# Kernel optimization log

Measured on AMD Instinct MI355X. Metric: run time of the kernel, lower is better.

## Reference

```python
import jax, jax.numpy as jnp
import numpy as np

N_NODES = 100000
N_EDGES = 3200000
R0, R1, R2, N1 = 16, 8, 16, 32


def setup_inputs() -> dict:
    key = jax.random.key(0)
    ks = jax.random.split(key, 12)
    x = jax.random.normal(ks[0], (N_NODES, R0), dtype=jnp.float32)
    edge_index = jax.random.randint(ks[1], (2, N_EDGES), 0, N_NODES, dtype=jnp.int64)
    s = 0.1
    return {
        "x": x,
        "edge_index": edge_index,
        # GraphConv 1: lin_rel (weight+bias) applied to aggregated neighbors, lin_root (no bias) to self
        "W_rel1": jax.random.normal(ks[2], (R0, R1), dtype=jnp.float32) * s,
        "b_rel1": jnp.zeros((R1,), dtype=jnp.float32),
        "W_root1": jax.random.normal(ks[3], (R0, R1), dtype=jnp.float32) * s,
        # GraphConv 2
        "W_rel2": jax.random.normal(ks[4], (R1, R2), dtype=jnp.float32) * s,
        "b_rel2": jnp.zeros((R2,), dtype=jnp.float32),
        "W_root2": jax.random.normal(ks[5], (R1, R2), dtype=jnp.float32) * s,
        # fc layers
        "W_fc1": jax.random.normal(ks[6], (R2, N1), dtype=jnp.float32) * s,
        "b_fc1": jnp.zeros((N1,), dtype=jnp.float32),
        "W_fc2": jax.random.normal(ks[7], (N1, 1), dtype=jnp.float32) * s,
        "b_fc2": jnp.zeros((1,), dtype=jnp.float32),
    }


def _graph_conv(x, src, dst, W_rel, b_rel, W_root):
    # GraphConv with aggr='add': out_i = lin_rel(sum_{j->i} x_j) + lin_root(x_i)
    agg = jax.ops.segment_sum(x[src], dst, num_segments=N_NODES)  # [N, d_in]
    return agg @ W_rel + b_rel + x @ W_root


def reference(x, edge_index,
              W_rel1, b_rel1, W_root1,
              W_rel2, b_rel2, W_root2,
              W_fc1, b_fc1, W_fc2, b_fc2):
    src, dst = edge_index[0], edge_index[1]
    h = jax.nn.relu(_graph_conv(x, src, dst, W_rel1, b_rel1, W_root1))
    h = jax.nn.relu(_graph_conv(h, src, dst, W_rel2, b_rel2, W_root2))
    h = jax.nn.relu(h @ W_fc1 + b_fc1)
    out = h @ W_fc2 + b_fc2  # [N, 1]
    return out - jnp.mean(out)
```

## Files before the change

kernel.cpp:

```cpp
#include <hip/hip_runtime.h>

#define NN 100000
#define NE 3200000
#define BSH 7
#define BNODES 128
#define NBUCK 782
#define BCAP 4800
#define BIN_CHUNK 8192
#define NBIN_BLOCKS ((NE + BIN_CHUNK - 1) / BIN_CHUNK)
#define NL1_BLOCKS ((NN + 1023) / 1024)
#define NAGG_BLOCKS 1568

#define S1 2097152.0f
#define S2 524288.0f
#define INV_S1 (1.0f / S1)
#define INV_S2 (1.0f / S2)

__global__ __launch_bounds__(1024, 8) void bin_and_l1(
        const float* __restrict__ x,
        const float* __restrict__ Wrel1,
        const float* __restrict__ brel1,
        const float* __restrict__ Wroot1,
        const int* __restrict__ src,
        const int* __restrict__ dst,
        int* __restrict__ y1q,
        int* __restrict__ initq,
        int* __restrict__ bucketCnt,
        int* __restrict__ bpay) {
    int t = threadIdx.x;

    if (blockIdx.x >= NBIN_BLOCKS) {
        __shared__ float sW[16 * 8];
        __shared__ float sR[16 * 8];
        __shared__ float sb[8];
        if (t < 128) { sW[t] = Wrel1[t]; sR[t] = Wroot1[t]; }
        if (t < 8)   { sb[t] = brel1[t]; }
        __syncthreads();

        int i = (blockIdx.x - NBIN_BLOCKS) * 1024 + t;
        if (i >= NN) return;

        const float4* xp = (const float4*)(x + (size_t)i * 16);
        float4 x0 = xp[0], x1 = xp[1], x2 = xp[2], x3 = xp[3];
        float xi[16] = {x0.x, x0.y, x0.z, x0.w, x1.x, x1.y, x1.z, x1.w,
                        x2.x, x2.y, x2.z, x2.w, x3.x, x3.y, x3.z, x3.w};

        float y[8], r[8];
#pragma unroll
        for (int j = 0; j < 8; ++j) { y[j] = 0.0f; r[j] = sb[j]; }
#pragma unroll
        for (int k = 0; k < 16; ++k) {
            float xv = xi[k];
#pragma unroll
            for (int j = 0; j < 8; ++j) {
                y[j] = fmaf(xv, sW[k * 8 + j], y[j]);
                r[j] = fmaf(xv, sR[k * 8 + j], r[j]);
            }
        }
        int4* yp = (int4*)(y1q + (size_t)i * 8);
        int4* ap = (int4*)(initq + (size_t)i * 8);
        int4 q0, q1, p0, p1;
        q0.x = __float2int_rn(y[0] * S1); q0.y = __float2int_rn(y[1] * S1);
        q0.z = __float2int_rn(y[2] * S1); q0.w = __float2int_rn(y[3] * S1);
        q1.x = __float2int_rn(y[4] * S1); q1.y = __float2int_rn(y[5] * S1);
        q1.z = __float2int_rn(y[6] * S1); q1.w = __float2int_rn(y[7] * S1);
        p0.x = __float2int_rn(r[0] * S1); p0.y = __float2int_rn(r[1] * S1);
        p0.z = __float2int_rn(r[2] * S1); p0.w = __float2int_rn(r[3] * S1);
        p1.x = __float2int_rn(r[4] * S1); p1.y = __float2int_rn(r[5] * S1);
        p1.z = __float2int_rn(r[6] * S1); p1.w = __float2int_rn(r[7] * S1);
        yp[0] = q0; yp[1] = q1;
        ap[0] = p0; ap[1] = p1;
        return;
    }

    __shared__ int2 stage2[BIN_CHUNK];
    __shared__ int  hist[NBUCK];
    __shared__ int  gdelta[NBUCK];
    __shared__ int  wsum16[16];

    int e0 = blockIdx.x * BIN_CHUNK;
    int nE = NE - e0; if (nE > BIN_CHUNK) nE = BIN_CHUNK;
    int nv = nE >> 2;

    if (t < NBUCK) hist[t] = 0;
    __syncthreads();

    const int4* dst4 = (const int4*)(dst + e0);
    const int4* src4 = (const int4*)(src + e0);

    int4 d0_, s0_, d1_, s1_;
    bool h0 = (t < nv), h1 = (t + 1024 < nv);
    if (h0) {
        d0_ = dst4[t]; s0_ = src4[t];
        atomicAdd(&hist[d0_.x >> BSH], 1);
        atomicAdd(&hist[d0_.y >> BSH], 1);
        atomicAdd(&hist[d0_.z >> BSH], 1);
        atomicAdd(&hist[d0_.w >> BSH], 1);
    }
    if (h1) {
        d1_ = dst4[t + 1024]; s1_ = src4[t + 1024];
        atomicAdd(&hist[d1_.x >> BSH], 1);
        atomicAdd(&hist[d1_.y >> BSH], 1);
        atomicAdd(&hist[d1_.z >> BSH], 1);
        atomicAdd(&hist[d1_.w >> BSH], 1);
    }
    __syncthreads();

    int c = (t < NBUCK) ? hist[t] : 0;
    int lane = t & 63, w = t >> 6;
    int pref = c;
#pragma unroll
    for (int off = 1; off < 64; off <<= 1) {
        int u = __shfl_up(pref, off);
        if (lane >= off) pref += u;
    }
    if (lane == 63) wsum16[w] = pref;
    __syncthreads();
    if (t < 16) {
        int s = wsum16[t];
#pragma unroll
        for (int off = 1; off < 16; off <<= 1) {
            int u = __shfl_up(s, off);
            if (t >= off) s += u;
        }
        wsum16[t] = s;
    }
    __syncthreads();
    int base = w ? wsum16[w - 1] : 0;
    int excl = base + pref - c;

    if (t < NBUCK) {
        int gb0 = c ? atomicAdd(&bucketCnt[t], c) : 0;
        hist[t] = excl;
        gdelta[t] = t * BCAP + gb0 - excl;
    }
    __syncthreads();

#define PLACE1(dv, sv) do {                                              \
        int b_ = (dv) >> BSH;                                            \
        int r_ = atomicAdd(&hist[b_], 1);                                \
        int ga_ = r_ + gdelta[b_];                                       \
        int2 e_; e_.x = (((dv) & (BNODES - 1)) << 17) | (sv);            \
        e_.y = (ga_ < (b_ + 1) * BCAP) ? ga_ : -1;                       \
        stage2[r_] = e_;                                                 \
    } while (0)

    if (h0) { PLACE1(d0_.x, s0_.x); PLACE1(d0_.y, s0_.y);
              PLACE1(d0_.z, s0_.z); PLACE1(d0_.w, s0_.w); }
    if (h1) { PLACE1(d1_.x, s1_.x); PLACE1(d1_.y, s1_.y);
              PLACE1(d1_.z, s1_.z); PLACE1(d1_.w, s1_.w); }
#undef PLACE1
    __syncthreads();

    for (int p = t; p < nE; p += 1024) {
        int2 e = stage2[p];
        if (e.y >= 0) bpay[e.y] = e.x;
    }
}

__global__ __launch_bounds__(512, 8) void bucket_agg1(const int* __restrict__ bucketCnt,
                                                      const int* __restrict__ bpay,
                                                      const int* __restrict__ y1q,
                                                      int* __restrict__ h1q ) {
    __shared__ int qacc[BNODES * 4];
    int t = threadIdx.x;
    int j = blockIdx.x & 15, kk = blockIdx.x >> 4;
    int b = (kk << 3) + (j & 7);
    int fh4 = (j >> 3) << 2;
    if (b >= NBUCK) return;
    int gb = b * BCAP;
    int fbase = b * (BNODES * 8);

    {
        int node = t >> 2, f = t & 3;
        int gi = fbase + node * 8 + fh4 + f;
        qacc[t] = (gi < NN * 8) ? h1q[gi] : 0;
    }
    int C = bucketCnt[b]; if (C > BCAP) C = BCAP;
    __syncthreads();

    int f = t & 3, g = t >> 2;
    const int4* bp4 = (const int4*)(bpay + gb);
    int iters = C >> 10;
    for (int it = 0; it < iters; ++it) {
        int4 va = bp4[(it << 8) + (g << 1)];
        int4 vb = bp4[(it << 8) + (g << 1) + 1];
        int a0 = y1q[((va.x & 0x1FFFF) << 3) + fh4 + f];
        int a1 = y1q[((va.y & 0x1FFFF) << 3) + fh4 + f];
        int a2 = y1q[((va.z & 0x1FFFF) << 3) + fh4 + f];
        int a3 = y1q[((va.w & 0x1FFFF) << 3) + fh4 + f];
        int a4 = y1q[((vb.x & 0x1FFFF) << 3) + fh4 + f];
        int a5 = y1q[((vb.y & 0x1FFFF) << 3) + fh4 + f];
        int a6 = y1q[((vb.z & 0x1FFFF) << 3) + fh4 + f];
        int a7 = y1q[((vb.w & 0x1FFFF) << 3) + fh4 + f];
        atomicAdd(&qacc[((va.x >> 17) << 2) + f], a0);
        atomicAdd(&qacc[((va.y >> 17) << 2) + f], a1);
        atomicAdd(&qacc[((va.z >> 17) << 2) + f], a2);
        atomicAdd(&qacc[((va.w >> 17) << 2) + f], a3);
        atomicAdd(&qacc[((vb.x >> 17) << 2) + f], a4);
        atomicAdd(&qacc[((vb.y >> 17) << 2) + f], a5);
        atomicAdd(&qacc[((vb.z >> 17) << 2) + f], a6);
        atomicAdd(&qacc[((vb.w >> 17) << 2) + f], a7);
    }
    for (int e = (iters << 10) + g; e < C; e += 128) {
        int v = bpay[gb + e];
        int a = y1q[((v & 0x1FFFF) << 3) + fh4 + f];
        atomicAdd(&qacc[((v >> 17) << 2) + f], a);
    }
    __syncthreads();

    {
        int node = t >> 2, fo = t & 3;
        int gi = fbase + node * 8 + fh4 + fo;
        if (gi < NN * 8) {
            float h = (float)qacc[t] * INV_S1;
            h = h > 0.0f ? h : 0.0f;
            h1q[gi] = __float2int_rn(h * S2);
        }
    }
}

__global__ __launch_bounds__(512, 8) void bucket_agg2(const int* __restrict__ bucketCnt,
                                                      const int* __restrict__ bpay,
                                                      const int* __restrict__ h1q,
                                                      int* __restrict__ sagg) {
    __shared__ int qacc[BNODES * 4];
    int t = threadIdx.x;
    int j = blockIdx.x & 15, kk = blockIdx.x >> 4;
    int b = (kk << 3) + (j & 7);
    int fh4 = (j >> 3) << 2;
    if (b >= NBUCK) return;
    int gb = b * BCAP;
    int fbase = b * (BNODES * 8);

    qacc[t] = 0;
    int C = bucketCnt[b]; if (C > BCAP) C = BCAP;
    __syncthreads();

    int f = t & 3, g = t >> 2;
    const int4* bp4 = (const int4*)(bpay + gb);
    int iters = C >> 10;
    for (int it = 0; it < iters; ++it) {
        int4 va = bp4[(it << 8) + (g << 1)];
        int4 vb = bp4[(it << 8) + (g << 1) + 1];
        int a0 = h1q[((va.x & 0x1FFFF) << 3) + fh4 + f];
        int a1 = h1q[((va.y & 0x1FFFF) << 3) + fh4 + f];
        int a2 = h1q[((va.z & 0x1FFFF) << 3) + fh4 + f];
        int a3 = h1q[((va.w & 0x1FFFF) << 3) + fh4 + f];
        int a4 = h1q[((vb.x & 0x1FFFF) << 3) + fh4 + f];
        int a5 = h1q[((vb.y & 0x1FFFF) << 3) + fh4 + f];
        int a6 = h1q[((vb.z & 0x1FFFF) << 3) + fh4 + f];
        int a7 = h1q[((vb.w & 0x1FFFF) << 3) + fh4 + f];
        atomicAdd(&qacc[((va.x >> 17) << 2) + f], a0);
        atomicAdd(&qacc[((va.y >> 17) << 2) + f], a1);
        atomicAdd(&qacc[((va.z >> 17) << 2) + f], a2);
        atomicAdd(&qacc[((va.w >> 17) << 2) + f], a3);
        atomicAdd(&qacc[((vb.x >> 17) << 2) + f], a4);
        atomicAdd(&qacc[((vb.y >> 17) << 2) + f], a5);
        atomicAdd(&qacc[((vb.z >> 17) << 2) + f], a6);
        atomicAdd(&qacc[((vb.w >> 17) << 2) + f], a7);
    }
    for (int e = (iters << 10) + g; e < C; e += 128) {
        int v = bpay[gb + e];
        int a = h1q[((v & 0x1FFFF) << 3) + fh4 + f];
        atomicAdd(&qacc[((v >> 17) << 2) + f], a);
    }
    __syncthreads();

    {
        int node = t >> 2, fo = t & 3;
        int gi = fbase + node * 8 + fh4 + fo;
        if (gi < NN * 8) sagg[gi] = qacc[t];
    }
}

__global__ __launch_bounds__(512) void dense_tail(const int* __restrict__ h1q,
                                                  const int* __restrict__ sagg,
                                                  const float* __restrict__ Wrel2,
                                                  const float* __restrict__ brel2,
                                                  const float* __restrict__ Wroot2,
                                                  const float* __restrict__ Wfc1,
                                                  const float* __restrict__ bfc1,
                                                  const float* __restrict__ Wfc2,
                                                  const float* __restrict__ bfc2,
                                                  float* __restrict__ out,
                                                  float* __restrict__ gsum) {
    __shared__ float sWrel2[128], sWroot2[128], sbrel2[16];
    __shared__ float sWfc1[512], sbfc1[32], sWfc2[32];
    __shared__ float sbfc2;
    __shared__ float wsum[8];

    int t = threadIdx.x;
    sWfc1[t] = Wfc1[t];
    if (t < 128) { sWrel2[t] = Wrel2[t]; sWroot2[t] = Wroot2[t]; }
    if (t >= 128 && t < 144) sbrel2[t - 128] = brel2[t - 128];
    if (t >= 192 && t < 224) { sbfc1[t - 192] = bfc1[t - 192]; sWfc2[t - 192] = Wfc2[t - 192]; }
    if (t == 256) sbfc2 = bfc2[0];
    __syncthreads();

    int node = blockIdx.x * 512 + t;
    float o = 0.0f;
    if (node < NN) {
        const int4* hp = (const int4*)(h1q + (size_t)node * 8);
        const int4* sp = (const int4*)(sagg + (size_t)node * 8);
        int4 ha = hp[0], hb = hp[1];
        int4 sa = sp[0], sb = sp[1];
        float h1v[8] = {ha.x * INV_S2, ha.y * INV_S2, ha.z * INV_S2, ha.w * INV_S2,
                        hb.x * INV_S2, hb.y * INV_S2, hb.z * INV_S2, hb.w * INV_S2};
        float s2[8]  = {sa.x * INV_S2, sa.y * INV_S2, sa.z * INV_S2, sa.w * INV_S2,
                        sb.x * INV_S2, sb.y * INV_S2, sb.z * INV_S2, sb.w * INV_S2};

        float h2[16];
#pragma unroll
        for (int jj = 0; jj < 16; ++jj) h2[jj] = sbrel2[jj];
#pragma unroll
        for (int k = 0; k < 8; ++k) {
            float sv = s2[k], hv = h1v[k];
#pragma unroll
            for (int jj = 0; jj < 16; ++jj) {
                h2[jj] = fmaf(sv, sWrel2[k * 16 + jj], h2[jj]);
                h2[jj] = fmaf(hv, sWroot2[k * 16 + jj], h2[jj]);
            }
        }
#pragma unroll
        for (int jj = 0; jj < 16; ++jj) h2[jj] = h2[jj] > 0.0f ? h2[jj] : 0.0f;

        o = sbfc2;
#pragma unroll
        for (int m = 0; m < 32; ++m) {
            float a = sbfc1[m];
#pragma unroll
            for (int jj = 0; jj < 16; ++jj) a = fmaf(h2[jj], sWfc1[jj * 32 + m], a);
            a = a > 0.0f ? a : 0.0f;
            o = fmaf(a, sWfc2[m], o);
        }
        out[node] = o;
    }

    float v = o;
#pragma unroll
    for (int off = 32; off > 0; off >>= 1) v += __shfl_down(v, off);
    int lane = t & 63, w = t >> 6;
    if (lane == 0) wsum[w] = v;
    __syncthreads();
    if (t == 0) {
        float s = 0.0f;
#pragma unroll
        for (int k = 0; k < 8; ++k) s += wsum[k];
        atomicAdd(gsum, s);
    }
}

__global__ void subtract_mean(float* __restrict__ out,
                              const float* __restrict__ gsum) {
    int i = blockIdx.x * blockDim.x + threadIdx.x;
    if (i < NN) out[i] -= (*gsum) * (1.0f / (float)NN);
}

extern "C" void kernel_launch(void* const* d_in, const int* in_sizes, int n_in,
                              void* d_out, int out_size, void* d_ws, size_t ws_size,
                              hipStream_t stream) {
    const float* x      = (const float*)d_in[0];
    const int*   ei     = (const int*)d_in[1];
    const float* Wrel1  = (const float*)d_in[2];
    const float* brel1  = (const float*)d_in[3];
    const float* Wroot1 = (const float*)d_in[4];
    const float* Wrel2  = (const float*)d_in[5];
    const float* brel2  = (const float*)d_in[6];
    const float* Wroot2 = (const float*)d_in[7];
    const float* Wfc1   = (const float*)d_in[8];
    const float* bfc1   = (const float*)d_in[9];
    const float* Wfc2   = (const float*)d_in[10];
    const float* bfc2   = (const float*)d_in[11];
    float* out = (float*)d_out;
    float* ws  = (float*)d_ws;

    int*   y1q       = (int*)ws;
    int*   h1q       = (int*)(ws + 800000);
    int*   bucketCnt = (int*)(ws + 1600000);
    float* gsum      = ws + 1600782;
    int*   bpay      = (int*)(ws + 1600783);
    int*   sagg      = y1q;

    const int* src = ei;
    const int* dst = ei + NE;

    hipMemsetAsync(bucketCnt, 0, (NBUCK + 1) * sizeof(int), stream);
    bin_and_l1<<<NBIN_BLOCKS + NL1_BLOCKS, 1024, 0, stream>>>(x, Wrel1, brel1, Wroot1,
                                                              src, dst, y1q, h1q,
                                                              bucketCnt, bpay);
    bucket_agg1<<<NAGG_BLOCKS, 512, 0, stream>>>(bucketCnt, bpay, y1q, h1q);
    bucket_agg2<<<NAGG_BLOCKS, 512, 0, stream>>>(bucketCnt, bpay, h1q, sagg);
    dense_tail<<<(NN + 511) / 512, 512, 0, stream>>>(h1q, sagg,
                                                     Wrel2, brel2, Wroot2,
                                                     Wfc1, bfc1, Wfc2, bfc2, out, gsum);
    subtract_mean<<<(NN + 255) / 256, 256, 0, stream>>>(out, gsum);
}
```

Before: 193.6 us.

## Split bucket edge ranges across block pairs with global atomic merge

Each aggregation block now handles all 8 features of a bucket but only half of its edge chunks, instead of half the features over all edges. Partial sums from shared memory are merged into global buffers with atomicAdd, and the relu-requantize step moves into a separate elementwise kernel that also zeroes the layer-2 accumulator. The aim is to read each edge payload once per bucket and gather contiguous 8-int rows per source node, improving locality. The cost is an extra kernel launch, global atomics, and the sagg buffer, which aliases y1q, having to be cleared between the two aggregations.

```diff
diff --git a/kernel.cpp b/kernel.cpp
--- a/kernel.cpp
+++ b/kernel.cpp
@@ -9,7 +9,7 @@
 #define BIN_CHUNK 8192
 #define NBIN_BLOCKS ((NE + BIN_CHUNK - 1) / BIN_CHUNK)
 #define NL1_BLOCKS ((NN + 1023) / 1024)
-#define NAGG_BLOCKS 1568
+#define NAGG_HALF (NBUCK * 2)
 
 #define S1 2097152.0f
 #define S2 524288.0f
@@ -158,119 +158,113 @@
     }
 }
 
-__global__ __launch_bounds__(512, 8) void bucket_agg1(const int* __restrict__ bucketCnt,
-                                                      const int* __restrict__ bpay,
-                                                      const int* __restrict__ y1q,
-                                                      int* __restrict__ h1q ) {
-    __shared__ int qacc[BNODES * 4];
+#define AGG_GATHER_LOOP(SRCBUF)                                              \
+    int f = t & 7, g = t >> 3;                                               \
+    const int4* bp4 = (const int4*)(bpay + gb);                              \
+    int iters = C >> 10;                                                     \
+    int it0 = h ? ((iters + 1) >> 1) : 0;                                    \
+    int it1 = h ? iters : ((iters + 1) >> 1);                                \
+    for (int it = it0; it < it1; ++it) {                                     \
+        int4 va = bp4[(it << 8) + (g << 2)];                                 \
+        int4 vb = bp4[(it << 8) + (g << 2) + 1];                             \
+        int4 vc = bp4[(it << 8) + (g << 2) + 2];                             \
+        int4 vd = bp4[(it << 8) + (g << 2) + 3];                             \
+        int a0 = SRCBUF[((va.x & 0x1FFFF) << 3) + f];                        \
+        int a1 = SRCBUF[((va.y & 0x1FFFF) << 3) + f];                        \
+        int a2 = SRCBUF[((va.z & 0x1FFFF) << 3) + f];                        \
+        int a3 = SRCBUF[((va.w & 0x1FFFF) << 3) + f];                        \
+        int a4 = SRCBUF[((vb.x & 0x1FFFF) << 3) + f];                        \
+        int a5 = SRCBUF[((vb.y & 0x1FFFF) << 3) + f];                        \
+        int a6 = SRCBUF[((vb.z & 0x1FFFF) << 3) + f];                        \
+        int a7 = SRCBUF[((vb.w & 0x1FFFF) << 3) + f];                        \
+        int a8 = SRCBUF[((vc.x & 0x1FFFF) << 3) + f];                        \
+        int a9 = SRCBUF[((vc.y & 0x1FFFF) << 3) + f];                        \
+        int aa = SRCBUF[((vc.z & 0x1FFFF) << 3) + f];                        \
+        int ab = SRCBUF[((vc.w & 0x1FFFF) << 3) + f];                        \
+        int ac = SRCBUF[((vd.x & 0x1FFFF) << 3) + f];                        \
+        int ad = SRCBUF[((vd.y & 0x1FFFF) << 3) + f];                        \
+        int ae = SRCBUF[((vd.z & 0x1FFFF) << 3) + f];                        \
+        int af = SRCBUF[((vd.w & 0x1FFFF) << 3) + f];                        \
+        atomicAdd(&qacc[((va.x >> 17) << 3) + f], a0);                       \
+        atomicAdd(&qacc[((va.y >> 17) << 3) + f], a1);                       \
+        atomicAdd(&qacc[((va.z >> 17) << 3) + f], a2);                       \
+        atomicAdd(&qacc[((va.w >> 17) << 3) + f], a3);                       \
+        atomicAdd(&qacc[((vb.x >> 17) << 3) + f], a4);                       \
+        atomicAdd(&qacc[((vb.y >> 17) << 3) + f], a5);                       \
+        atomicAdd(&qacc[((vb.z >> 17) << 3) + f], a6);                       \
+        atomicAdd(&qacc[((vb.w >> 17) << 3) + f], a7);                       \
+        atomicAdd(&qacc[((vc.x >> 17) << 3) + f], a8);                       \
+        atomicAdd(&qacc[((vc.y >> 17) << 3) + f], a9);                       \
+        atomicAdd(&qacc[((vc.z >> 17) << 3) + f], aa);                       \
+        atomicAdd(&qacc[((vc.w >> 17) << 3) + f], ab);                       \
+        atomicAdd(&qacc[((vd.x >> 17) << 3) + f], ac);                       \
+        atomicAdd(&qacc[((vd.y >> 17) << 3) + f], ad);                       \
+        atomicAdd(&qacc[((vd.z >> 17) << 3) + f], ae);                       \
+        atomicAdd(&qacc[((vd.w >> 17) << 3) + f], af);                       \
+    }                                                                        \
+    if (h) {                                                                 \
+        for (int e = (iters << 10) + g; e < C; e += 64) {                    \
+            int v = bpay[gb + e];                                            \
+            int a = SRCBUF[((v & 0x1FFFF) << 3) + f];                        \
+            atomicAdd(&qacc[((v >> 17) << 3) + f], a);                       \
+        }                                                                    \
+    }
+
+__global__ __launch_bounds__(512, 8) void bucket_agg1_half(const int* __restrict__ bucketCnt,
+                                                           const int* __restrict__ bpay,
+                                                           const int* __restrict__ y1q,
+                                                           int* __restrict__ h1q ) {
+    __shared__ int qacc[BNODES * 8];
     int t = threadIdx.x;
-    int j = blockIdx.x & 15, kk = blockIdx.x >> 4;
-    int b = (kk << 3) + (j & 7);
-    int fh4 = (j >> 3) << 2;
-    if (b >= NBUCK) return;
+    int b = blockIdx.x >> 1, h = blockIdx.x & 1;
     int gb = b * BCAP;
     int fbase = b * (BNODES * 8);
 
-    {
-        int node = t >> 2, f = t & 3;
-        int gi = fbase + node * 8 + fh4 + f;
-        qacc[t] = (gi < NN * 8) ? h1q[gi] : 0;
-    }
+    qacc[t] = 0; qacc[t + 512] = 0;
     int C = bucketCnt[b]; if (C > BCAP) C = BCAP;
     __syncthreads();
 
-    int f = t & 3, g = t >> 2;
-    const int4* bp4 = (const int4*)(bpay + gb);
-    int iters = C >> 10;
-    for (int it = 0; it < iters; ++it) {
-        int4 va = bp4[(it << 8) + (g << 1)];
-        int4 vb = bp4[(it << 8) + (g << 1) + 1];
-        int a0 = y1q[((va.x & 0x1FFFF) << 3) + fh4 + f];
-        int a1 = y1q[((va.y & 0x1FFFF) << 3) + fh4 + f];
-        int a2 = y1q[((va.z & 0x1FFFF) << 3) + fh4 + f];
-        int a3 = y1q[((va.w & 0x1FFFF) << 3) + fh4 + f];
-        int a4 = y1q[((vb.x & 0x1FFFF) << 3) + fh4 + f];
-        int a5 = y1q[((vb.y & 0x1FFFF) << 3) + fh4 + f];
-        int a6 = y1q[((vb.z & 0x1FFFF) << 3) + fh4 + f];
-        int a7 = y1q[((vb.w & 0x1FFFF) << 3) + fh4 + f];
-        atomicAdd(&qacc[((va.x >> 17) << 2) + f], a0);
-        atomicAdd(&qacc[((va.y >> 17) << 2) + f], a1);
-        atomicAdd(&qacc[((va.z >> 17) << 2) + f], a2);
-        atomicAdd(&qacc[((va.w >> 17) << 2) + f], a3);
-        atomicAdd(&qacc[((vb.x >> 17) << 2) + f], a4);
-        atomicAdd(&qacc[((vb.y >> 17) << 2) + f], a5);
-        atomicAdd(&qacc[((vb.z >> 17) << 2) + f], a6);
-        atomicAdd(&qacc[((vb.w >> 17) << 2) + f], a7);
-    }
-    for (int e = (iters << 10) + g; e < C; e += 128) {
-        int v = bpay[gb + e];
-        int a = y1q[((v & 0x1FFFF) << 3) + fh4 + f];
-        atomicAdd(&qacc[((v >> 17) << 2) + f], a);
-    }
-    __syncthreads();
-
-    {
-        int node = t >> 2, fo = t & 3;
-        int gi = fbase + node * 8 + fh4 + fo;
-        if (gi < NN * 8) {
-            float h = (float)qacc[t] * INV_S1;
-            h = h > 0.0f ? h : 0.0f;
-            h1q[gi] = __float2int_rn(h * S2);
-        }
-    }
-}
-
-__global__ __launch_bounds__(512, 8) void bucket_agg2(const int* __restrict__ bucketCnt,
-                                                      const int* __restrict__ bpay,
-                                                      const int* __restrict__ h1q,
-                                                      int* __restrict__ sagg) {
-    __shared__ int qacc[BNODES * 4];
+    AGG_GATHER_LOOP(y1q)
+    __syncthreads();
+
+    for (int k = t; k < BNODES * 8; k += 512) {
+        int gi = fbase + k;
+        int v = qacc[k];
+        if (gi < NN * 8 && v != 0) atomicAdd(&h1q[gi], v);
+    }
+}
+
+__global__ void relu_quant_zero(int* __restrict__ h1q, int* __restrict__ sagg) {
+    int i = blockIdx.x * 1024 + threadIdx.x;
+    if (i < NN * 8) {
+        float hv = (float)h1q[i] * INV_S1;
+        hv = hv > 0.0f ? hv : 0.0f;
+        h1q[i] = __float2int_rn(hv * S2);
+        sagg[i] = 0;
+    }
+}
+
+__global__ __launch_bounds__(512, 8) void bucket_agg2_half(const int* __restrict__ bucketCnt,
+                                                           const int* __restrict__ bpay,
+                                                           const int* __restrict__ h1q,
+                                                           int* __restrict__ sagg) {
+    __shared__ int qacc[BNODES * 8];
     int t = threadIdx.x;
-    int j = blockIdx.x & 15, kk = blockIdx.x >> 4;
-    int b = (kk << 3) + (j & 7);
-    int fh4 = (j >> 3) << 2;
-    if (b >= NBUCK) return;
+    int b = blockIdx.x >> 1, h = blockIdx.x & 1;
     int gb = b * BCAP;
     int fbase = b * (BNODES * 8);
 
-    qacc[t] = 0;
+    qacc[t] = 0; qacc[t + 512] = 0;
     int C = bucketCnt[b]; if (C > BCAP) C = BCAP;
     __syncthreads();
 
-    int f = t & 3, g = t >> 2;
-    const int4* bp4 = (const int4*)(bpay + gb);
-    int iters = C >> 10;
-    for (int it = 0; it < iters; ++it) {
-        int4 va = bp4[(it << 8) + (g << 1)];
-        int4 vb = bp4[(it << 8) + (g << 1) + 1];
-        int a0 = h1q[((va.x & 0x1FFFF) << 3) + fh4 + f];
-        int a1 = h1q[((va.y & 0x1FFFF) << 3) + fh4 + f];
-        int a2 = h1q[((va.z & 0x1FFFF) << 3) + fh4 + f];
-        int a3 = h1q[((va.w & 0x1FFFF) << 3) + fh4 + f];
-        int a4 = h1q[((vb.x & 0x1FFFF) << 3) + fh4 + f];
-        int a5 = h1q[((vb.y & 0x1FFFF) << 3) + fh4 + f];
-        int a6 = h1q[((vb.z & 0x1FFFF) << 3) + fh4 + f];
-        int a7 = h1q[((vb.w & 0x1FFFF) << 3) + fh4 + f];
-        atomicAdd(&qacc[((va.x >> 17) << 2) + f], a0);
-        atomicAdd(&qacc[((va.y >> 17) << 2) + f], a1);
-        atomicAdd(&qacc[((va.z >> 17) << 2) + f], a2);
-        atomicAdd(&qacc[((va.w >> 17) << 2) + f], a3);
-        atomicAdd(&qacc[((vb.x >> 17) << 2) + f], a4);
-        atomicAdd(&qacc[((vb.y >> 17) << 2) + f], a5);
-        atomicAdd(&qacc[((vb.z >> 17) << 2) + f], a6);
-        atomicAdd(&qacc[((vb.w >> 17) << 2) + f], a7);
-    }
-    for (int e = (iters << 10) + g; e < C; e += 128) {
-        int v = bpay[gb + e];
-        int a = h1q[((v & 0x1FFFF) << 3) + fh4 + f];
-        atomicAdd(&qacc[((v >> 17) << 2) + f], a);
-    }
-    __syncthreads();
-
-    {
-        int node = t >> 2, fo = t & 3;
-        int gi = fbase + node * 8 + fh4 + fo;
-        if (gi < NN * 8) sagg[gi] = qacc[t];
+    AGG_GATHER_LOOP(h1q)
+    __syncthreads();
+
+    for (int k = t; k < BNODES * 8; k += 512) {
+        int gi = fbase + k;
+        int v = qacc[k];
+        if (gi < NN * 8 && v != 0) atomicAdd(&sagg[gi], v);
     }
 }
 
@@ -389,8 +383,9 @@
     bin_and_l1<<<NBIN_BLOCKS + NL1_BLOCKS, 1024, 0, stream>>>(x, Wrel1, brel1, Wroot1,
                                                               src, dst, y1q, h1q,
                                                               bucketCnt, bpay);
-    bucket_agg1<<<NAGG_BLOCKS, 512, 0, stream>>>(bucketCnt, bpay, y1q, h1q);
-    bucket_agg2<<<NAGG_BLOCKS, 512, 0, stream>>>(bucketCnt, bpay, h1q, sagg);
+    bucket_agg1_half<<<NAGG_HALF, 512, 0, stream>>>(bucketCnt, bpay, y1q, h1q);
+    relu_quant_zero<<<(NN * 8 + 1023) / 1024, 1024, 0, stream>>>(h1q, sagg);
+    bucket_agg2_half<<<NAGG_HALF, 512, 0, stream>>>(bucketCnt, bpay, h1q, sagg);
     dense_tail<<<(NN + 511) / 512, 512, 0, stream>>>(h1q, sagg,
                                                      Wrel2, brel2, Wroot2,
                                                      Wfc1, bfc1, Wfc2, bfc2, out, gsum);
```

Measured after the change: 176.0 us. 1.1x faster.
